# Optimization experiments

Hardware: AMD Instinct MI355X
Metric: run time of the kernel (lower is better)

The kernel has to match this reference:

```python
import jax, jax.numpy as jnp
import numpy as np


def setup_inputs() -> dict:
    key = jax.random.key(0)
    k1, k2, k3 = jax.random.split(key, 3)
    B, OUT, IN = 256, 512, 512
    x = jax.random.normal(k1, (B, IN), dtype=jnp.float32)
    weight = jax.random.normal(k2, (OUT, IN), dtype=jnp.float32)
    logits = jax.random.normal(k3, (OUT, IN), dtype=jnp.float32)
    return {"x": x, "weight": weight, "logits": logits}


def reference(x, weight, logits):
    # x: [B, IN]; weight/logits: [OUT, IN]
    B = x.shape[0]
    OUT, IN = logits.shape
    kg1, kg2 = jax.random.split(jax.random.key(42))

    # weight property: 2*tanh(_weight) * gumbel_softmax(_logits, hard=True), tau=1
    g1 = jax.random.gumbel(kg1, (OUT, IN), dtype=logits.dtype)
    soft1 = jax.nn.softmax(logits + g1, axis=-1)
    hard1 = jax.nn.one_hot(jnp.argmax(soft1, axis=-1), IN, dtype=soft1.dtype)
    # straight-through: forward value is the one-hot
    mask_hard = hard1 + soft1 - jax.lax.stop_gradient(soft1)
    W_eff = 2.0 * jnp.tanh(2.0 * jnp.tanh(weight) * mask_hard)  # [OUT, IN]

    # per-example soft gumbel-softmax mask over the in-dim, tau=1
    g2 = jax.random.gumbel(kg2, (B, OUT, IN), dtype=logits.dtype)
    L = jax.nn.softmax(logits[None, :, :] + g2, axis=-1)  # [B, OUT, IN]

    # y[b,o] = sum_i W_eff[o,i] * L[b,o,i] * x[b,i]
    y = jnp.einsum('oi,boi,bi->bo', W_eff, L, x)
    return y
```

## Files before the change

### kernel.cpp

```cpp
#include <hip/hip_runtime.h>
#include <stdint.h>


__device__ __forceinline__ float fast_log2(float x) {
  float r; asm("v_log_f32 %0, %1" : "=v"(r) : "v"(x)); return r;
}
__device__ __forceinline__ float fast_exp2(float x) {
  float r; asm("v_exp_f32 %0, %1" : "=v"(r) : "v"(x)); return r;
}
__device__ __forceinline__ float fast_tanh(float w) {
  float t = fast_exp2(w * 2.8853900817779268f);
  return (t - 1.0f) / (t + 1.0f);
}

#if defined(__has_builtin) && __has_builtin(__builtin_amdgcn_alignbit)
__device__ __forceinline__ uint32_t rotl_ab(uint32_t x, int r) {
  return __builtin_amdgcn_alignbit(x, x, 32u - (unsigned)r);
}
#else
__device__ __forceinline__ uint32_t rotl_ab(uint32_t x, int r) {
  uint32_t d;
  asm("v_alignbit_b32 %0, %1, %1, %2" : "=v"(d) : "v"(x), "v"(32u - (unsigned)r));
  return d;
}
#endif

__device__ __forceinline__ void threefry2x32(uint32_t k0, uint32_t k1,
                                             uint32_t x0, uint32_t x1,
                                             uint32_t& o0, uint32_t& o1) {
  const uint32_t ks2 = k0 ^ k1 ^ 0x1BD11BDAu;
  x0 += k0; x1 += k1;
#define TF_RND(r) { x0 += x1; x1 = rotl_ab(x1, (r)); x1 ^= x0; }
  TF_RND(13) TF_RND(15) TF_RND(26) TF_RND(6)
  x0 += k1;  x1 += ks2 + 1u;
  TF_RND(17) TF_RND(29) TF_RND(16) TF_RND(24)
  x0 += ks2; x1 += k0 + 2u;
  TF_RND(13) TF_RND(15) TF_RND(26) TF_RND(6)
  x0 += k0;  x1 += k1 + 3u;
  TF_RND(17) TF_RND(29) TF_RND(16) TF_RND(24)
  x0 += k1;  x1 += ks2 + 4u;
  TF_RND(13) TF_RND(15) TF_RND(26) TF_RND(6)
  x0 += ks2; x1 += k0 + 5u;
#undef TF_RND
  o0 = x0; o1 = x1;
}

__device__ __forceinline__ uint32_t tf_bits(uint32_t ka, uint32_t kb, uint32_t e) {
  uint32_t r0, r1;
  threefry2x32(ka, kb, 0u, e, r0, r1);
  return r0 ^ r1;
}

__device__ __forceinline__ float neglog2_from_bits(uint32_t bits) {
  float f  = __uint_as_float((bits >> 9) | 0x3f800000u) - 1.0f;
  float l1 = fast_log2(f);
  float nl = fmaxf(-l1, 1e-37f);
  return fast_log2(nl);
}

__global__ __launch_bounds__(256) void k_fused(const float* __restrict__ x,
                                               const float* __restrict__ weight,
                                               const float* __restrict__ logits,
                                               float* __restrict__ out) {
  const int o    = blockIdx.x & 511;
  const int bg   = blockIdx.x >> 9;
  const int tid  = threadIdx.x;
  const int lane = tid & 63;
  const int wid  = tid >> 6;
  const float* lrow = logits + o * 512;

  uint32_t k1a, k1b, k2a, k2b;
  threefry2x32(0u, 42u, 0u, 0u, k1a, k1b);
  threefry2x32(0u, 42u, 0u, 1u, k2a, k2b);

  float v; int idx;
  {
    const uint32_t e0 = (uint32_t)(o * 512 + tid);
    float g1a = fmaf(-0.69314718056f, neglog2_from_bits(tf_bits(k1a, k1b, e0)),
                     0.3665129206f);
    v   = lrow[tid] + g1a;
    idx = tid;
    float g1b = fmaf(-0.69314718056f, neglog2_from_bits(tf_bits(k1a, k1b, e0 + 256u)),
                     0.3665129206f);
    float v2 = lrow[tid + 256] + g1b;
    if (v2 > v) { v = v2; idx = tid + 256; }
  }
  for (int off = 32; off > 0; off >>= 1) {
    float ov = __shfl_down(v, off);
    int   oi = __shfl_down(idx, off);
    if (ov > v || (ov == v && oi < idx)) { v = ov; idx = oi; }
  }
  __shared__ float swv[4];
  __shared__ int   swi[4];
  __shared__ int   s_istar;
  __shared__ float s_c;
  if (lane == 0) { swv[wid] = v; swi[wid] = idx; }
  __syncthreads();
  if (tid == 0) {
    float bv = swv[0]; int bi = swi[0];
    for (int w = 1; w < 4; ++w)
      if (swv[w] > bv || (swv[w] == bv && swi[w] < bi)) { bv = swv[w]; bi = swi[w]; }
    s_istar = bi;
    s_c = 2.0f * fast_tanh(2.0f * fast_tanh(weight[o * 512 + bi]));
  }
  __syncthreads();
  const int   isel = s_istar;
  const float c    = s_c;

  float lsc0 = fmaf(lrow[lane      ], 1.4426950408889634f, 0.5287663729f);
  float lsc1 = fmaf(lrow[lane +  64], 1.4426950408889634f, 0.5287663729f);
  float lsc2 = fmaf(lrow[lane + 128], 1.4426950408889634f, 0.5287663729f);
  float lsc3 = fmaf(lrow[lane + 192], 1.4426950408889634f, 0.5287663729f);
  float lsc4 = fmaf(lrow[lane + 256], 1.4426950408889634f, 0.5287663729f);
  float lsc5 = fmaf(lrow[lane + 320], 1.4426950408889634f, 0.5287663729f);
  float lsc6 = fmaf(lrow[lane + 384], 1.4426950408889634f, 0.5287663729f);
  float lsc7 = fmaf(lrow[lane + 448], 1.4426950408889634f, 0.5287663729f);

  const bool hit0 = (lane       == isel);
  const bool hit1 = (lane +  64 == isel);
  const bool hit2 = (lane + 128 == isel);
  const bool hit3 = (lane + 192 == isel);
  const bool hit4 = (lane + 256 == isel);
  const bool hit5 = (lane + 320 == isel);
  const bool hit6 = (lane + 384 == isel);
  const bool hit7 = (lane + 448 == isel);

  const int b0 = bg * 64 + wid * 16;
#pragma unroll 1
  for (int it = 0; it < 16; ++it) {
    const int b   = b0 + it;
    const int row = (b << 9) | o;
    const uint32_t base = (uint32_t)row << 9;
    const uint32_t elane = base + (uint32_t)lane;

    float sum = 0.0f, selv = 0.0f;
#define G2_SAMPLE(J, LSC, HIT)                                    \
    {                                                             \
      float l2 = neglog2_from_bits(tf_bits(k2a, k2b, elane + 64u * (J))); \
      float ev = fast_exp2((LSC) - l2);                           \
      sum += ev;                                                  \
      selv = (HIT) ? ev : selv;                                   \
    }
    G2_SAMPLE(0, lsc0, hit0) G2_SAMPLE(1, lsc1, hit1)
    G2_SAMPLE(2, lsc2, hit2) G2_SAMPLE(3, lsc3, hit3)
    G2_SAMPLE(4, lsc4, hit4) G2_SAMPLE(5, lsc5, hit5)
    G2_SAMPLE(6, lsc6, hit6) G2_SAMPLE(7, lsc7, hit7)
#undef G2_SAMPLE
    for (int off = 32; off > 0; off >>= 1) sum += __shfl_down(sum, off);
    selv = __shfl(selv, isel & 63);
    if (lane == 0) out[row] = c * x[(b << 9) | isel] * selv / sum;
  }
}

extern "C" void kernel_launch(void* const* d_in, const int* in_sizes, int n_in,
                              void* d_out, int out_size, void* d_ws, size_t ws_size,
                              hipStream_t stream) {
  const float* x      = (const float*)d_in[0];
  const float* weight = (const float*)d_in[1];
  const float* logits = (const float*)d_in[2];
  float* out = (float*)d_out;
  k_fused<<<dim3(512 * 4), dim3(256), 0, stream>>>(x, weight, logits, out);
}
```

Baseline: 181.1 us.

## Constant-fold threefry keys, hand-schedule paired rounds, replace exp/log with rcp

Computes the threefry subkeys at compile time and passes them as scalar constants. The hot threefry path becomes a hand-written asm block that interleaves two independent streams. Its first round is simplified because x0 starts at zero, and the rotation amounts are expressed as alignbit shifts. The softmax term exp(l - log(-log u)) is rewritten as exp(l) * 1/(-log u), with exp(l) hoisted out of the loop. This drops one log and one exp per sample in favour of a single rcp. The rcp, the algebraic rewrite and the hand-coded asm can change rounding slightly and need careful correctness checks.

```diff
diff --git a/kernel.cpp b/kernel.cpp
--- a/kernel.cpp
+++ b/kernel.cpp
@@ -2,35 +2,106 @@
 #include <stdint.h>
 
 
+struct U2 { uint32_t a, b; };
+constexpr uint32_t crotl(uint32_t x, int r) { return (x << r) | (x >> (32 - r)); }
+
+constexpr U2 ctf(uint32_t k0, uint32_t k1, uint32_t x0, uint32_t x1) {
+  const uint32_t ks2 = k0 ^ k1 ^ 0x1BD11BDAu;
+  x0 += k0; x1 += k1;
+  x0 += x1; x1 = crotl(x1, 13); x1 ^= x0;
+  x0 += x1; x1 = crotl(x1, 15); x1 ^= x0;
+  x0 += x1; x1 = crotl(x1, 26); x1 ^= x0;
+  x0 += x1; x1 = crotl(x1, 6);  x1 ^= x0;
+  x0 += k1;  x1 += ks2 + 1u;
+  x0 += x1; x1 = crotl(x1, 17); x1 ^= x0;
+  x0 += x1; x1 = crotl(x1, 29); x1 ^= x0;
+  x0 += x1; x1 = crotl(x1, 16); x1 ^= x0;
+  x0 += x1; x1 = crotl(x1, 24); x1 ^= x0;
+  x0 += ks2; x1 += k0 + 2u;
+  x0 += x1; x1 = crotl(x1, 13); x1 ^= x0;
+  x0 += x1; x1 = crotl(x1, 15); x1 ^= x0;
+  x0 += x1; x1 = crotl(x1, 26); x1 ^= x0;
+  x0 += x1; x1 = crotl(x1, 6);  x1 ^= x0;
+  x0 += k0;  x1 += k1 + 3u;
+  x0 += x1; x1 = crotl(x1, 17); x1 ^= x0;
+  x0 += x1; x1 = crotl(x1, 29); x1 ^= x0;
+  x0 += x1; x1 = crotl(x1, 16); x1 ^= x0;
+  x0 += x1; x1 = crotl(x1, 24); x1 ^= x0;
+  x0 += k1;  x1 += ks2 + 4u;
+  x0 += x1; x1 = crotl(x1, 13); x1 ^= x0;
+  x0 += x1; x1 = crotl(x1, 15); x1 ^= x0;
+  x0 += x1; x1 = crotl(x1, 26); x1 ^= x0;
+  x0 += x1; x1 = crotl(x1, 6);  x1 ^= x0;
+  x0 += ks2; x1 += k0 + 5u;
+  return U2{x0, x1};
+}
+
+constexpr U2 KG1 = ctf(0u, 42u, 0u, 0u);
+constexpr U2 KG2 = ctf(0u, 42u, 0u, 1u);
+constexpr uint32_t K0  = KG2.a, K1 = KG2.b;
+constexpr uint32_t KS2 = K0 ^ K1 ^ 0x1BD11BDAu;
+constexpr uint32_t C1 = KS2 + 1u, C2 = K0 + 2u, C3 = K1 + 3u,
+                   C4 = KS2 + 4u, C5 = K0 + 5u;
+
+#define TFR2(S) \
+  "v_add_u32 %0,%0,%1\n\t" "v_add_u32 %2,%2,%3\n\t" \
+  "v_alignbit_b32 %1,%1,%1," S "\n\t" "v_alignbit_b32 %3,%3,%3," S "\n\t" \
+  "v_xor_b32 %1,%1,%0\n\t" "v_xor_b32 %3,%3,%2\n\t"
+#define INJ2(KA, KB) \
+  "v_add_u32 %0," KA ",%0\n\t" "v_add_u32 %2," KA ",%2\n\t" \
+  "v_add_u32 %1," KB ",%1\n\t" "v_add_u32 %3," KB ",%3\n\t"
+
+__device__ __forceinline__ void tf20x2(uint32_t x1a, uint32_t x1b,
+                                       uint32_t& ba, uint32_t& bb) {
+  uint32_t x0a, x0b;
+  asm(
+      "v_add_u32 %0,%4,%1\n\t" "v_add_u32 %2,%4,%3\n\t"
+      "v_alignbit_b32 %1,%1,%1,19\n\t" "v_alignbit_b32 %3,%3,%3,19\n\t"
+      "v_xor_b32 %1,%1,%0\n\t" "v_xor_b32 %3,%3,%2\n\t"
+      TFR2("17") TFR2("6") TFR2("26")
+      INJ2("%5", "%7")
+      TFR2("15") TFR2("3") TFR2("16") TFR2("8")
+      INJ2("%6", "%8")
+      TFR2("19") TFR2("17") TFR2("6") TFR2("26")
+      INJ2("%4", "%9")
+      TFR2("15") TFR2("3") TFR2("16") TFR2("8")
+      INJ2("%5", "%10")
+      TFR2("19") TFR2("17") TFR2("6") TFR2("26")
+      INJ2("%6", "%11")
+      "v_xor_b32 %1,%1,%0\n\t" "v_xor_b32 %3,%3,%2\n\t"
+      : "=&v"(x0a), "+v"(x1a), "=&v"(x0b), "+v"(x1b)
+      : "s"(K0), "s"(K1), "s"(KS2), "s"(C1), "s"(C2), "s"(C3), "s"(C4), "s"(C5));
+  ba = x1a; bb = x1b;
+}
+
 __device__ __forceinline__ float fast_log2(float x) {
   float r; asm("v_log_f32 %0, %1" : "=v"(r) : "v"(x)); return r;
 }
 __device__ __forceinline__ float fast_exp2(float x) {
   float r; asm("v_exp_f32 %0, %1" : "=v"(r) : "v"(x)); return r;
 }
+#if defined(__has_builtin) && __has_builtin(__builtin_amdgcn_rcpf)
+__device__ __forceinline__ float rcp_neg(float x) {
+  return __builtin_amdgcn_rcpf(-x);
+}
+#else
+__device__ __forceinline__ float rcp_neg(float x) {
+  float r; asm("v_rcp_f32_e64 %0, -%1" : "=v"(r) : "v"(x)); return r;
+}
+#endif
 __device__ __forceinline__ float fast_tanh(float w) {
   float t = fast_exp2(w * 2.8853900817779268f);
   return (t - 1.0f) / (t + 1.0f);
 }
 
-#if defined(__has_builtin) && __has_builtin(__builtin_amdgcn_alignbit)
-__device__ __forceinline__ uint32_t rotl_ab(uint32_t x, int r) {
-  return __builtin_amdgcn_alignbit(x, x, 32u - (unsigned)r);
-}
-#else
-__device__ __forceinline__ uint32_t rotl_ab(uint32_t x, int r) {
-  uint32_t d;
-  asm("v_alignbit_b32 %0, %1, %1, %2" : "=v"(d) : "v"(x), "v"(32u - (unsigned)r));
-  return d;
-}
-#endif
-
-__device__ __forceinline__ void threefry2x32(uint32_t k0, uint32_t k1,
-                                             uint32_t x0, uint32_t x1,
-                                             uint32_t& o0, uint32_t& o1) {
+__device__ __forceinline__ uint32_t rotl(uint32_t x, int r) {
+  return __builtin_rotateleft32(x, (unsigned)r);
+}
+__device__ __forceinline__ uint32_t tf_bits_g1(uint32_t e) {
+  const uint32_t k0 = KG1.a, k1 = KG1.b;
   const uint32_t ks2 = k0 ^ k1 ^ 0x1BD11BDAu;
-  x0 += k0; x1 += k1;
-#define TF_RND(r) { x0 += x1; x1 = rotl_ab(x1, (r)); x1 ^= x0; }
+  uint32_t x0 = k0, x1 = e + k1;
+#define TF_RND(r) { x0 += x1; x1 = rotl(x1, (r)); x1 ^= x0; }
   TF_RND(13) TF_RND(15) TF_RND(26) TF_RND(6)
   x0 += k1;  x1 += ks2 + 1u;
   TF_RND(17) TF_RND(29) TF_RND(16) TF_RND(24)
@@ -42,15 +113,8 @@
   TF_RND(13) TF_RND(15) TF_RND(26) TF_RND(6)
   x0 += ks2; x1 += k0 + 5u;
 #undef TF_RND
-  o0 = x0; o1 = x1;
-}
-
-__device__ __forceinline__ uint32_t tf_bits(uint32_t ka, uint32_t kb, uint32_t e) {
-  uint32_t r0, r1;
-  threefry2x32(ka, kb, 0u, e, r0, r1);
-  return r0 ^ r1;
-}
-
+  return x0 ^ x1;
+}
 __device__ __forceinline__ float neglog2_from_bits(uint32_t bits) {
   float f  = __uint_as_float((bits >> 9) | 0x3f800000u) - 1.0f;
   float l1 = fast_log2(f);
@@ -69,18 +133,14 @@
   const int wid  = tid >> 6;
   const float* lrow = logits + o * 512;
 
-  uint32_t k1a, k1b, k2a, k2b;
-  threefry2x32(0u, 42u, 0u, 0u, k1a, k1b);
-  threefry2x32(0u, 42u, 0u, 1u, k2a, k2b);
-
   float v; int idx;
   {
     const uint32_t e0 = (uint32_t)(o * 512 + tid);
-    float g1a = fmaf(-0.69314718056f, neglog2_from_bits(tf_bits(k1a, k1b, e0)),
+    float g1a = fmaf(-0.69314718056f, neglog2_from_bits(tf_bits_g1(e0)),
                      0.3665129206f);
     v   = lrow[tid] + g1a;
     idx = tid;
-    float g1b = fmaf(-0.69314718056f, neglog2_from_bits(tf_bits(k1a, k1b, e0 + 256u)),
+    float g1b = fmaf(-0.69314718056f, neglog2_from_bits(tf_bits_g1(e0 + 256u)),
                      0.3665129206f);
     float v2 = lrow[tid + 256] + g1b;
     if (v2 > v) { v = v2; idx = tid + 256; }
@@ -107,14 +167,15 @@
   const int   isel = s_istar;
   const float c    = s_c;
 
-  float lsc0 = fmaf(lrow[lane      ], 1.4426950408889634f, 0.5287663729f);
-  float lsc1 = fmaf(lrow[lane +  64], 1.4426950408889634f, 0.5287663729f);
-  float lsc2 = fmaf(lrow[lane + 128], 1.4426950408889634f, 0.5287663729f);
-  float lsc3 = fmaf(lrow[lane + 192], 1.4426950408889634f, 0.5287663729f);
-  float lsc4 = fmaf(lrow[lane + 256], 1.4426950408889634f, 0.5287663729f);
-  float lsc5 = fmaf(lrow[lane + 320], 1.4426950408889634f, 0.5287663729f);
-  float lsc6 = fmaf(lrow[lane + 384], 1.4426950408889634f, 0.5287663729f);
-  float lsc7 = fmaf(lrow[lane + 448], 1.4426950408889634f, 0.5287663729f);
+  const float LOG2E = 1.4426950408889634f, CADD = 0.5287663729f;
+  float el0 = fast_exp2(fmaf(lrow[lane      ], LOG2E, CADD));
+  float el1 = fast_exp2(fmaf(lrow[lane +  64], LOG2E, CADD));
+  float el2 = fast_exp2(fmaf(lrow[lane + 128], LOG2E, CADD));
+  float el3 = fast_exp2(fmaf(lrow[lane + 192], LOG2E, CADD));
+  float el4 = fast_exp2(fmaf(lrow[lane + 256], LOG2E, CADD));
+  float el5 = fast_exp2(fmaf(lrow[lane + 320], LOG2E, CADD));
+  float el6 = fast_exp2(fmaf(lrow[lane + 384], LOG2E, CADD));
+  float el7 = fast_exp2(fmaf(lrow[lane + 448], LOG2E, CADD));
 
   const bool hit0 = (lane       == isel);
   const bool hit1 = (lane +  64 == isel);
@@ -131,21 +192,25 @@
     const int b   = b0 + it;
     const int row = (b << 9) | o;
     const uint32_t base = (uint32_t)row << 9;
-    const uint32_t elane = base + (uint32_t)lane;
+    const uint32_t ekrow = base + (uint32_t)lane + K1;
 
     float sum = 0.0f, selv = 0.0f;
-#define G2_SAMPLE(J, LSC, HIT)                                    \
-    {                                                             \
-      float l2 = neglog2_from_bits(tf_bits(k2a, k2b, elane + 64u * (J))); \
-      float ev = fast_exp2((LSC) - l2);                           \
-      sum += ev;                                                  \
-      selv = (HIT) ? ev : selv;                                   \
+#define G2_PAIR(JA, ELA, HA, ELB, HB)                                \
+    {                                                                \
+      uint32_t bA, bB;                                               \
+      tf20x2(ekrow + 128u * (JA), ekrow + 128u * (JA) + 64u, bA, bB);\
+      float fA = __uint_as_float((bA >> 9) | 0x3f800000u) - 1.0f;    \
+      float fB = __uint_as_float((bB >> 9) | 0x3f800000u) - 1.0f;    \
+      float evA = (ELA) * rcp_neg(fast_log2(fA));                    \
+      float evB = (ELB) * rcp_neg(fast_log2(fB));                    \
+      sum += evA; selv = (HA) ? evA : selv;                          \
+      sum += evB; selv = (HB) ? evB : selv;                          \
     }
-    G2_SAMPLE(0, lsc0, hit0) G2_SAMPLE(1, lsc1, hit1)
-    G2_SAMPLE(2, lsc2, hit2) G2_SAMPLE(3, lsc3, hit3)
-    G2_SAMPLE(4, lsc4, hit4) G2_SAMPLE(5, lsc5, hit5)
-    G2_SAMPLE(6, lsc6, hit6) G2_SAMPLE(7, lsc7, hit7)
-#undef G2_SAMPLE
+    G2_PAIR(0, el0, hit0, el1, hit1)
+    G2_PAIR(1, el2, hit2, el3, hit3)
+    G2_PAIR(2, el4, hit4, el5, hit5)
+    G2_PAIR(3, el6, hit6, el7, hit7)
+#undef G2_PAIR
     for (int off = 32; off > 0; off >>= 1) sum += __shfl_down(sum, off);
     selv = __shfl(selv, isel & 63);
     if (lane == 0) out[row] = c * x[(b << 9) | isel] * selv / sum;
```

Result: faster. 154.4 us (-14.7%).
